# Performance work log

Hardware: AMD Instinct MI355X
Metric: run time of the kernel (lower is better)

## Reference

```python
import jax, jax.numpy as jnp
import numpy as np

E, B, S, H = 8, 16, 512, 1024
LN_EPS = 1e-12


def setup_inputs() -> dict:
    key = jax.random.key(0)
    k = jax.random.split(key, 5)
    return {
        "hidden_states": jax.random.normal(k[0], (B, S, H), dtype=jnp.float32),
        "input_tensor": jax.random.normal(k[1], (B, S, H), dtype=jnp.float32),
        "expert_idx": jax.random.randint(k[2], (B,), 0, E, dtype=jnp.int64)
        if jax.config.jax_enable_x64 else jax.random.randint(k[2], (B,), 0, E, dtype=jnp.int32),
        "W": jax.random.normal(k[3], (E, H, H), dtype=jnp.float32) * (1.0 / np.sqrt(H)),
        "b": jax.random.normal(k[4], (E, H), dtype=jnp.float32) * 0.02,
        "gamma": jnp.ones((H,), dtype=jnp.float32),
        "beta": jnp.zeros((H,), dtype=jnp.float32),
    }


def reference(hidden_states, input_tensor, expert_idx, W, b, gamma, beta):
    # All-expert dense forward, matching single_select_fwd's stacked compute.
    # all_out: [E, B, S, H]
    all_out = jnp.einsum("bsh,ehd->ebsd", hidden_states, W) + b[:, None, None, :]
    # slice_for_expert: pick (expert_idx[b], b) for each batch row -> [B, S, H]
    selected = all_out[expert_idx, jnp.arange(hidden_states.shape[0])]
    # dropout is identity in eval mode; residual + LayerNorm
    x = selected + input_tensor
    mu = jnp.mean(x, axis=-1, keepdims=True)
    var = jnp.mean(jnp.square(x - mu), axis=-1, keepdims=True)
    return (x - mu) * jax.lax.rsqrt(var + LN_EPS) * gamma + beta
```

## Files before the change

### kernel.cpp

```cpp
#include <hip/hip_runtime.h>
#include <hip/hip_bf16.h>

#define BB 16
#define SS 512
#define HH 1024

typedef __attribute__((ext_vector_type(4))) float f32x4;
typedef __attribute__((ext_vector_type(8))) short bhalf8;

static __device__ __forceinline__ unsigned int pack2(float a, float b) {
    __hip_bfloat162 h = __float22bfloat162_rn(make_float2(a, b));
    union { __hip_bfloat162 h; unsigned int u; } cv;
    cv.h = h;
    return cv.u;
}

__global__ __launch_bounds__(256)
void prep_kernel(const float* __restrict__ W, const float* __restrict__ hid,
                 const int* __restrict__ eidx, unsigned short* __restrict__ Wt,
                 unsigned short* __restrict__ hidb)
{
    int bid = blockIdx.x;
    int t = threadIdx.x;
    if (bid < 2048) {
        __shared__ float lds[32 * 132];
        int e  = bid >> 8;
        bool used = false;
        for (int b = 0; b < BB; ++b) used = used || (eidx[b] == e);
        if (!used) return;
        int rem = bid & 255;
        int kt = rem >> 3, dt = rem & 7;
#pragma unroll
        for (int i = 0; i < 4; ++i) {
            int idx = t + i * 256;
            int row = idx >> 5, col4 = idx & 31;
            float4 v = *(const float4*)(W + ((size_t)e << 20)
                        + (size_t)(kt * 32 + row) * HH + dt * 128 + col4 * 4);
            float* dst = &lds[row * 132 + col4 * 4];
            dst[0] = v.x; dst[1] = v.y; dst[2] = v.z; dst[3] = v.w;
        }
        __syncthreads();
        int d = t >> 1, kh = t & 1;
        unsigned int u[8];
#pragma unroll
        for (int p = 0; p < 8; ++p) {
            float a = lds[(kh * 16 + p * 2)     * 132 + d];
            float b = lds[(kh * 16 + p * 2 + 1) * 132 + d];
            u[p] = pack2(a, b);
        }
        unsigned short* dst = Wt + ((size_t)e << 20)
                            + (size_t)(dt * 128 + d) * HH + kt * 32 + kh * 16;
        *reinterpret_cast<uint4*>(dst)     = make_uint4(u[0], u[1], u[2], u[3]);
        *reinterpret_cast<uint4*>(dst + 8) = make_uint4(u[4], u[5], u[6], u[7]);
    } else {
        int bid2 = bid - 2048;
        int r = bid2 * 2 + (t >> 7);
        int col = (t & 127) * 8;
        const float* src = hid + (size_t)r * HH + col;
        float4 v0 = *(const float4*)(src);
        float4 v1 = *(const float4*)(src + 4);
        uint4 o;
        o.x = pack2(v0.x, v0.y); o.y = pack2(v0.z, v0.w);
        o.z = pack2(v1.x, v1.y); o.w = pack2(v1.z, v1.w);
        *reinterpret_cast<uint4*>(hidb + (size_t)r * HH + col) = o;
    }
}

__global__ __launch_bounds__(512, 2)
void gemm8_kernel(const unsigned short* __restrict__ hidb,
                  const int* __restrict__ eidx,
                  const unsigned short* __restrict__ Wt,
                  float* __restrict__ out)
{
    __shared__ char ldsA[4 * 16384];
    __shared__ char ldsW[4 * 8192];

    int bx  = blockIdx.x;
    int swz = (bx & 7) * 32 + (bx >> 3);
    int bt   = swz >> 4;
    int tile = swz & 15;
    int mt = tile >> 3, nt = tile & 7;
    int e = eidx[bt];

    int t = threadIdx.x, wave = t >> 6, lane = t & 63;
    int l15 = lane & 15, g = lane >> 4;
    int wm = wave >> 1, wn = wave & 1;

    int brow = bt * SS + mt * 256;
    int ncol0 = nt * 128;

    const unsigned short* asrc[2];
    int aoff[2];
#pragma unroll
    for (int i = 0; i < 2; ++i) {
        int c = t + i * 512;
        int line = c >> 3, p = c & 7, q = p ^ (line & 7);
        int row = line * 2 + (q >> 2), s = q & 3;
        asrc[i] = hidb + (size_t)(brow + row) * HH + s * 8;
        aoff[i] = c * 16;
    }
    const unsigned short* wsrc;
    int woff;
    {
        int line = t >> 3, p = t & 7, q = p ^ (line & 7);
        int row = line * 2 + (q >> 2), s = q & 3;
        wsrc = Wt + ((size_t)e << 20) + (size_t)(ncol0 + row) * HH + s * 8;
        woff = t * 16;
    }

    auto stage = [&](int ks, int b) {
#pragma unroll
        for (int i = 0; i < 2; ++i)
            __builtin_amdgcn_global_load_lds(
                (const __attribute__((address_space(1))) void*)(asrc[i] + ks * 32),
                (__attribute__((address_space(3))) void*)(ldsA + b * 16384 + aoff[i]),
                16, 0, 0);
        __builtin_amdgcn_global_load_lds(
            (const __attribute__((address_space(1))) void*)(wsrc + ks * 32),
            (__attribute__((address_space(3))) void*)(ldsW + b * 8192 + woff),
            16, 0, 0);
    };

    f32x4 acc[4][4] = {};

    auto body = [&](int ks, bool do_stage) {
        const char* Af = ldsA + (ks & 3) * 16384;
        const char* Wf = ldsW + (ks & 3) * 8192;
        bhalf8 af[4], bf[4];
#pragma unroll
        for (int mf = 0; mf < 4; ++mf) {
            int r = wm * 64 + mf * 16 + l15;
            int line = r >> 1;
            int p = (g + ((r & 1) << 2)) ^ (line & 7);
            af[mf] = *reinterpret_cast<const bhalf8*>(Af + line * 128 + p * 16);
        }
#pragma unroll
        for (int nf = 0; nf < 4; ++nf) {
            int d = wn * 64 + nf * 16 + l15;
            int line = d >> 1;
            int p = (g + ((d & 1) << 2)) ^ (line & 7);
            bf[nf] = *reinterpret_cast<const bhalf8*>(Wf + line * 128 + p * 16);
        }
        if (do_stage) stage(ks + 3, (ks + 3) & 3);
        __builtin_amdgcn_s_barrier();
        __builtin_amdgcn_s_setprio(1);
#pragma unroll
        for (int mf = 0; mf < 4; ++mf)
#pragma unroll
            for (int nf = 0; nf < 4; ++nf)
                acc[mf][nf] = __builtin_amdgcn_mfma_f32_16x16x32_bf16(
                    af[mf], bf[nf], acc[mf][nf], 0, 0, 0);
        __builtin_amdgcn_s_setprio(0);
    };

    stage(0, 0); stage(1, 1); stage(2, 2);
    asm volatile("s_waitcnt vmcnt(6)" ::: "memory");
    __builtin_amdgcn_s_barrier();

    for (int ks = 0; ks < 29; ++ks) {
        body(ks, true);
        asm volatile("s_waitcnt vmcnt(6)" ::: "memory");
        __builtin_amdgcn_s_barrier();
    }
    body(29, false);
    asm volatile("s_waitcnt vmcnt(3)" ::: "memory");
    __builtin_amdgcn_s_barrier();
    body(30, false);
    asm volatile("s_waitcnt vmcnt(0)" ::: "memory");
    __builtin_amdgcn_s_barrier();
    body(31, false);

#pragma unroll
    for (int nf = 0; nf < 4; ++nf) {
        int dcol = ncol0 + wn * 64 + nf * 16 + l15;
#pragma unroll
        for (int mf = 0; mf < 4; ++mf)
#pragma unroll
            for (int j = 0; j < 4; ++j) {
                int srow = brow + wm * 64 + mf * 16 + g * 4 + j;
                out[(size_t)srow * HH + dcol] = acc[mf][nf][j];
            }
    }
}

__global__ __launch_bounds__(256)
void post_kernel(float* __restrict__ y, const float* __restrict__ inp,
                 const int* __restrict__ eidx, const float* __restrict__ bias,
                 const float* __restrict__ gamma, const float* __restrict__ beta)
{
    int bid = blockIdx.x;
    int row = ((bid & 7) << 10) | (bid >> 3);
    int bt = row >> 9;
    int e = eidx[bt];
    int t = threadIdx.x;

    size_t base = (size_t)row * HH + t * 4;
    float4 v  = *reinterpret_cast<const float4*>(&y[base]);
    float4 iv = *reinterpret_cast<const float4*>(&inp[base]);
    float4 bv = *reinterpret_cast<const float4*>(&bias[e * HH + t * 4]);
    float4 x;
    x.x = v.x + iv.x + bv.x;
    x.y = v.y + iv.y + bv.y;
    x.z = v.z + iv.z + bv.z;
    x.w = v.w + iv.w + bv.w;

    float s1 = x.x + x.y + x.z + x.w;
    float s2 = x.x * x.x + x.y * x.y + x.z * x.z + x.w * x.w;
#pragma unroll
    for (int off = 32; off > 0; off >>= 1) {
        s1 += __shfl_xor(s1, off, 64);
        s2 += __shfl_xor(s2, off, 64);
    }
    __shared__ float red[8];
    if ((t & 63) == 0) { red[(t >> 6) * 2] = s1; red[(t >> 6) * 2 + 1] = s2; }
    __syncthreads();
    float S1 = red[0] + red[2] + red[4] + red[6];
    float S2 = red[1] + red[3] + red[5] + red[7];
    float mu  = S1 * (1.0f / HH);
    float var = S2 * (1.0f / HH) - mu * mu;
    float rs = rsqrtf(var + 1e-12f);

    float4 gv = *reinterpret_cast<const float4*>(&gamma[t * 4]);
    float4 be = *reinterpret_cast<const float4*>(&beta[t * 4]);
    float4 o;
    o.x = (x.x - mu) * rs * gv.x + be.x;
    o.y = (x.y - mu) * rs * gv.y + be.y;
    o.z = (x.z - mu) * rs * gv.z + be.z;
    o.w = (x.w - mu) * rs * gv.w + be.w;
    *reinterpret_cast<float4*>(&y[base]) = o;
}

extern "C" void kernel_launch(void* const* d_in, const int* in_sizes, int n_in,
                              void* d_out, int out_size, void* d_ws, size_t ws_size,
                              hipStream_t stream) {
    const float* hid   = (const float*)d_in[0];
    const float* inp   = (const float*)d_in[1];
    const int*   eidx  = (const int*)d_in[2];
    const float* W     = (const float*)d_in[3];
    const float* bias  = (const float*)d_in[4];
    const float* gamma = (const float*)d_in[5];
    const float* beta  = (const float*)d_in[6];
    float* out = (float*)d_out;

    unsigned short* Wt   = (unsigned short*)d_ws;
    unsigned short* hidb = (unsigned short*)((char*)d_ws + (16u << 20));

    prep_kernel<<<6144, 256, 0, stream>>>(W, hid, eidx, Wt, hidb);
    gemm8_kernel<<<256, 512, 0, stream>>>(hidb, eidx, Wt, out);
    post_kernel<<<BB * SS, 256, 0, stream>>>(out, inp, eidx, bias, gamma, beta);
}
```

Before: 60.89 us.

## Fuse bias and residual add into GEMM epilogue; issue prefetch before LDS reads

The GEMM epilogue now adds the selected expert's bias and the residual input before storing. The LayerNorm kernel therefore only reads the pre-normalised row plus gamma/beta, which removes its separate input and bias loads and the expert-index lookup. The main loop also issues the next tile's global-to-LDS load at the start of each iteration and drops the barrier between the fragment reads and the MFMAs. Both changes cut per-step synchronisation and post-kernel traffic, but the epilogue's residual reads follow the MFMA output layout and may coalesce less well.

```diff
diff --git a/kernel.cpp b/kernel.cpp
--- a/kernel.cpp
+++ b/kernel.cpp
@@ -68,8 +68,10 @@
 
 __global__ __launch_bounds__(512, 2)
 void gemm8_kernel(const unsigned short* __restrict__ hidb,
+                  const float* __restrict__ inp,
                   const int* __restrict__ eidx,
                   const unsigned short* __restrict__ Wt,
+                  const float* __restrict__ bias,
                   float* __restrict__ out)
 {
     __shared__ char ldsA[4 * 16384];
@@ -123,7 +125,7 @@
 
     f32x4 acc[4][4] = {};
 
-    auto body = [&](int ks, bool do_stage) {
+    auto body = [&](int ks) {
         const char* Af = ldsA + (ks & 3) * 16384;
         const char* Wf = ldsW + (ks & 3) * 8192;
         bhalf8 af[4], bf[4];
@@ -141,8 +143,6 @@
             int p = (g + ((d & 1) << 2)) ^ (line & 7);
             bf[nf] = *reinterpret_cast<const bhalf8*>(Wf + line * 128 + p * 16);
         }
-        if (do_stage) stage(ks + 3, (ks + 3) & 3);
-        __builtin_amdgcn_s_barrier();
         __builtin_amdgcn_s_setprio(1);
 #pragma unroll
         for (int mf = 0; mf < 4; ++mf)
@@ -157,55 +157,49 @@
     asm volatile("s_waitcnt vmcnt(6)" ::: "memory");
     __builtin_amdgcn_s_barrier();
 
-    for (int ks = 0; ks < 29; ++ks) {
-        body(ks, true);
-        asm volatile("s_waitcnt vmcnt(6)" ::: "memory");
-        __builtin_amdgcn_s_barrier();
-    }
-    body(29, false);
-    asm volatile("s_waitcnt vmcnt(3)" ::: "memory");
-    __builtin_amdgcn_s_barrier();
-    body(30, false);
-    asm volatile("s_waitcnt vmcnt(0)" ::: "memory");
-    __builtin_amdgcn_s_barrier();
-    body(31, false);
+    for (int ks = 0; ks < 32; ++ks) {
+        if (ks <= 28) stage(ks + 3, (ks + 3) & 3);
+        body(ks);
+        if (ks < 29) {
+            asm volatile("s_waitcnt vmcnt(6)" ::: "memory");
+            __builtin_amdgcn_s_barrier();
+        } else if (ks == 29) {
+            asm volatile("s_waitcnt vmcnt(3)" ::: "memory");
+            __builtin_amdgcn_s_barrier();
+        } else if (ks == 30) {
+            asm volatile("s_waitcnt vmcnt(0)" ::: "memory");
+            __builtin_amdgcn_s_barrier();
+        }
+    }
 
 #pragma unroll
     for (int nf = 0; nf < 4; ++nf) {
         int dcol = ncol0 + wn * 64 + nf * 16 + l15;
+        float bv = bias[e * HH + dcol];
 #pragma unroll
         for (int mf = 0; mf < 4; ++mf)
 #pragma unroll
             for (int j = 0; j < 4; ++j) {
                 int srow = brow + wm * 64 + mf * 16 + g * 4 + j;
-                out[(size_t)srow * HH + dcol] = acc[mf][nf][j];
+                size_t off = (size_t)srow * HH + dcol;
+                out[off] = acc[mf][nf][j] + bv + inp[off];
             }
     }
 }
 
 __global__ __launch_bounds__(256)
-void post_kernel(float* __restrict__ y, const float* __restrict__ inp,
-                 const int* __restrict__ eidx, const float* __restrict__ bias,
-                 const float* __restrict__ gamma, const float* __restrict__ beta)
+void post_kernel(float* __restrict__ x, const float* __restrict__ gamma,
+                 const float* __restrict__ beta)
 {
     int bid = blockIdx.x;
     int row = ((bid & 7) << 10) | (bid >> 3);
-    int bt = row >> 9;
-    int e = eidx[bt];
     int t = threadIdx.x;
 
     size_t base = (size_t)row * HH + t * 4;
-    float4 v  = *reinterpret_cast<const float4*>(&y[base]);
-    float4 iv = *reinterpret_cast<const float4*>(&inp[base]);
-    float4 bv = *reinterpret_cast<const float4*>(&bias[e * HH + t * 4]);
-    float4 x;
-    x.x = v.x + iv.x + bv.x;
-    x.y = v.y + iv.y + bv.y;
-    x.z = v.z + iv.z + bv.z;
-    x.w = v.w + iv.w + bv.w;
-
-    float s1 = x.x + x.y + x.z + x.w;
-    float s2 = x.x * x.x + x.y * x.y + x.z * x.z + x.w * x.w;
+    float4 v = *reinterpret_cast<const float4*>(&x[base]);
+
+    float s1 = v.x + v.y + v.z + v.w;
+    float s2 = v.x * v.x + v.y * v.y + v.z * v.z + v.w * v.w;
 #pragma unroll
     for (int off = 32; off > 0; off >>= 1) {
         s1 += __shfl_xor(s1, off, 64);
@@ -223,11 +217,11 @@
     float4 gv = *reinterpret_cast<const float4*>(&gamma[t * 4]);
     float4 be = *reinterpret_cast<const float4*>(&beta[t * 4]);
     float4 o;
-    o.x = (x.x - mu) * rs * gv.x + be.x;
-    o.y = (x.y - mu) * rs * gv.y + be.y;
-    o.z = (x.z - mu) * rs * gv.z + be.z;
-    o.w = (x.w - mu) * rs * gv.w + be.w;
-    *reinterpret_cast<float4*>(&y[base]) = o;
+    o.x = (v.x - mu) * rs * gv.x + be.x;
+    o.y = (v.y - mu) * rs * gv.y + be.y;
+    o.z = (v.z - mu) * rs * gv.z + be.z;
+    o.w = (v.w - mu) * rs * gv.w + be.w;
+    *reinterpret_cast<float4*>(&x[base]) = o;
 }
 
 extern "C" void kernel_launch(void* const* d_in, const int* in_sizes, int n_in,
@@ -246,6 +240,6 @@
     unsigned short* hidb = (unsigned short*)((char*)d_ws + (16u << 20));
 
     prep_kernel<<<6144, 256, 0, stream>>>(W, hid, eidx, Wt, hidb);
-    gemm8_kernel<<<256, 512, 0, stream>>>(hidb, eidx, Wt, out);
-    post_kernel<<<BB * SS, 256, 0, stream>>>(out, inp, eidx, bias, gamma, beta);
-}
+    gemm8_kernel<<<256, 512, 0, stream>>>(hidb, inp, eidx, Wt, bias, out);
+    post_kernel<<<BB * SS, 256, 0, stream>>>(out, gamma, beta);
+}
```

New measurement: 67.05 us (median of 2 runs). 1.1x slower.

## Fuse bias, residual and LayerNorm into GEMM epilogue via cross-block row sums

Applied to the files above, without the earlier changes.

Removes the separate post-processing kernel by folding bias and residual adds into the GEMM accumulators. Per-row sum and sum-of-squares are accumulated with global atomics across the 8 column tiles of each row panel, followed by a spin-wait barrier on a per-panel counter before normalising in registers. This saves the fp32 round-trip of the GEMM output plus a kernel launch. In exchange it relies on all 256 blocks being co-resident, since the inter-block spin could deadlock otherwise. The prep kernel gains extra blocks that zero the sums and counters.

```diff
diff --git a/kernel.cpp b/kernel.cpp
--- a/kernel.cpp
+++ b/kernel.cpp
@@ -18,7 +18,7 @@
 __global__ __launch_bounds__(256)
 void prep_kernel(const float* __restrict__ W, const float* __restrict__ hid,
                  const int* __restrict__ eidx, unsigned short* __restrict__ Wt,
-                 unsigned short* __restrict__ hidb)
+                 unsigned short* __restrict__ hidb, float* __restrict__ zero_base)
 {
     int bid = blockIdx.x;
     int t = threadIdx.x;
@@ -52,7 +52,7 @@
                             + (size_t)(dt * 128 + d) * HH + kt * 32 + kh * 16;
         *reinterpret_cast<uint4*>(dst)     = make_uint4(u[0], u[1], u[2], u[3]);
         *reinterpret_cast<uint4*>(dst + 8) = make_uint4(u[4], u[5], u[6], u[7]);
-    } else {
+    } else if (bid < 6144) {
         int bid2 = bid - 2048;
         int r = bid2 * 2 + (t >> 7);
         int col = (t & 127) * 8;
@@ -63,14 +63,26 @@
         o.x = pack2(v0.x, v0.y); o.y = pack2(v0.z, v0.w);
         o.z = pack2(v1.x, v1.y); o.w = pack2(v1.z, v1.w);
         *reinterpret_cast<uint4*>(hidb + (size_t)r * HH + col) = o;
+    } else {
+        int idx = (bid - 6144) * 1024 + t * 4;
+        if (idx < 16448) {
+            float4 z = {0.f, 0.f, 0.f, 0.f};
+            *reinterpret_cast<float4*>(&zero_base[idx]) = z;
+        }
     }
 }
 
 __global__ __launch_bounds__(512, 2)
-void gemm8_kernel(const unsigned short* __restrict__ hidb,
-                  const int* __restrict__ eidx,
-                  const unsigned short* __restrict__ Wt,
-                  float* __restrict__ out)
+void gemm_ln_kernel(const unsigned short* __restrict__ hidb,
+                    const float* __restrict__ inp,
+                    const int* __restrict__ eidx,
+                    const unsigned short* __restrict__ Wt,
+                    const float* __restrict__ bias,
+                    const float* __restrict__ gamma,
+                    const float* __restrict__ beta,
+                    float* __restrict__ sums,
+                    int* __restrict__ cnt,
+                    float* __restrict__ out)
 {
     __shared__ char ldsA[4 * 16384];
     __shared__ char ldsW[4 * 8192];
@@ -80,6 +92,7 @@
     int bt   = swz >> 4;
     int tile = swz & 15;
     int mt = tile >> 3, nt = tile & 7;
+    int panel = swz >> 3;
     int e = eidx[bt];
 
     int t = threadIdx.x, wave = t >> 6, lane = t & 63;
@@ -173,61 +186,70 @@
 #pragma unroll
     for (int nf = 0; nf < 4; ++nf) {
         int dcol = ncol0 + wn * 64 + nf * 16 + l15;
+        float bv = bias[e * HH + dcol];
 #pragma unroll
         for (int mf = 0; mf < 4; ++mf)
 #pragma unroll
             for (int j = 0; j < 4; ++j) {
                 int srow = brow + wm * 64 + mf * 16 + g * 4 + j;
-                out[(size_t)srow * HH + dcol] = acc[mf][nf][j];
-            }
-    }
-}
-
-__global__ __launch_bounds__(256)
-void post_kernel(float* __restrict__ y, const float* __restrict__ inp,
-                 const int* __restrict__ eidx, const float* __restrict__ bias,
-                 const float* __restrict__ gamma, const float* __restrict__ beta)
-{
-    int bid = blockIdx.x;
-    int row = ((bid & 7) << 10) | (bid >> 3);
-    int bt = row >> 9;
-    int e = eidx[bt];
-    int t = threadIdx.x;
-
-    size_t base = (size_t)row * HH + t * 4;
-    float4 v  = *reinterpret_cast<const float4*>(&y[base]);
-    float4 iv = *reinterpret_cast<const float4*>(&inp[base]);
-    float4 bv = *reinterpret_cast<const float4*>(&bias[e * HH + t * 4]);
-    float4 x;
-    x.x = v.x + iv.x + bv.x;
-    x.y = v.y + iv.y + bv.y;
-    x.z = v.z + iv.z + bv.z;
-    x.w = v.w + iv.w + bv.w;
-
-    float s1 = x.x + x.y + x.z + x.w;
-    float s2 = x.x * x.x + x.y * x.y + x.z * x.z + x.w * x.w;
-#pragma unroll
-    for (int off = 32; off > 0; off >>= 1) {
-        s1 += __shfl_xor(s1, off, 64);
-        s2 += __shfl_xor(s2, off, 64);
-    }
-    __shared__ float red[8];
-    if ((t & 63) == 0) { red[(t >> 6) * 2] = s1; red[(t >> 6) * 2 + 1] = s2; }
+                acc[mf][nf][j] += bv + inp[(size_t)srow * HH + dcol];
+            }
+    }
+
+#pragma unroll
+    for (int mf = 0; mf < 4; ++mf)
+#pragma unroll
+        for (int j = 0; j < 4; ++j) {
+            float s1 = 0.f, s2 = 0.f;
+#pragma unroll
+            for (int nf = 0; nf < 4; ++nf) {
+                float v = acc[mf][nf][j];
+                s1 += v; s2 += v * v;
+            }
+#pragma unroll
+            for (int m = 8; m >= 1; m >>= 1) {
+                s1 += __shfl_xor(s1, m, 64);
+                s2 += __shfl_xor(s2, m, 64);
+            }
+            if (l15 == 0) {
+                int r = brow + wm * 64 + mf * 16 + g * 4 + j;
+                atomicAdd(&sums[r * 2], s1);
+                atomicAdd(&sums[r * 2 + 1], s2);
+            }
+        }
+
+    __threadfence();
     __syncthreads();
-    float S1 = red[0] + red[2] + red[4] + red[6];
-    float S2 = red[1] + red[3] + red[5] + red[7];
-    float mu  = S1 * (1.0f / HH);
-    float var = S2 * (1.0f / HH) - mu * mu;
-    float rs = rsqrtf(var + 1e-12f);
-
-    float4 gv = *reinterpret_cast<const float4*>(&gamma[t * 4]);
-    float4 be = *reinterpret_cast<const float4*>(&beta[t * 4]);
-    float4 o;
-    o.x = (x.x - mu) * rs * gv.x + be.x;
-    o.y = (x.y - mu) * rs * gv.y + be.y;
-    o.z = (x.z - mu) * rs * gv.z + be.z;
-    o.w = (x.w - mu) * rs * gv.w + be.w;
-    *reinterpret_cast<float4*>(&y[base]) = o;
+    if (t == 0) {
+        __hip_atomic_fetch_add(&cnt[panel], 1, __ATOMIC_RELEASE, __HIP_MEMORY_SCOPE_AGENT);
+        while (__hip_atomic_load(&cnt[panel], __ATOMIC_ACQUIRE, __HIP_MEMORY_SCOPE_AGENT) < 8)
+            __builtin_amdgcn_s_sleep(4);
+    }
+    __syncthreads();
+
+    float gv[4], be[4];
+#pragma unroll
+    for (int nf = 0; nf < 4; ++nf) {
+        int dcol = ncol0 + wn * 64 + nf * 16 + l15;
+        gv[nf] = gamma[dcol];
+        be[nf] = beta[dcol];
+    }
+#pragma unroll
+    for (int mf = 0; mf < 4; ++mf)
+#pragma unroll
+        for (int j = 0; j < 4; ++j) {
+            int r = brow + wm * 64 + mf * 16 + g * 4 + j;
+            float s1 = __hip_atomic_load(&sums[r * 2],     __ATOMIC_RELAXED, __HIP_MEMORY_SCOPE_AGENT);
+            float s2 = __hip_atomic_load(&sums[r * 2 + 1], __ATOMIC_RELAXED, __HIP_MEMORY_SCOPE_AGENT);
+            float mu  = s1 * (1.0f / HH);
+            float var = s2 * (1.0f / HH) - mu * mu;
+            float rs = rsqrtf(var + 1e-12f);
+#pragma unroll
+            for (int nf = 0; nf < 4; ++nf) {
+                int dcol = ncol0 + wn * 64 + nf * 16 + l15;
+                out[(size_t)r * HH + dcol] = (acc[mf][nf][j] - mu) * rs * gv[nf] + be[nf];
+            }
+        }
 }
 
 extern "C" void kernel_launch(void* const* d_in, const int* in_sizes, int n_in,
@@ -244,8 +266,10 @@
 
     unsigned short* Wt   = (unsigned short*)d_ws;
     unsigned short* hidb = (unsigned short*)((char*)d_ws + (16u << 20));
-
-    prep_kernel<<<6144, 256, 0, stream>>>(W, hid, eidx, Wt, hidb);
-    gemm8_kernel<<<256, 512, 0, stream>>>(hidb, eidx, Wt, out);
-    post_kernel<<<BB * SS, 256, 0, stream>>>(out, inp, eidx, bias, gamma, beta);
-}
+    float* sums = (float*)((char*)d_ws + (32u << 20));
+    int*   cnt  = (int*)((char*)d_ws + (32u << 20) + 65536);
+
+    prep_kernel<<<6161, 256, 0, stream>>>(W, hid, eidx, Wt, hidb, sums);
+    gemm_ln_kernel<<<256, 512, 0, stream>>>(hidb, inp, eidx, Wt, bias, gamma,
+                                            beta, sums, cnt, out);
+}
```

New measurement: 100.8 us. 1.65x slower.
